# Kernel tuning notes

Hardware: AMD Instinct MI355X
Metric: run time of the kernel (lower is better)

Reference implementation:

```python
import jax, jax.numpy as jnp
import numpy as np

N_LEVELS = 2 ** 4 - 1  # 4-bit uniform quantization -> 15 intervals


def fake_quant(x, lower, upper):
    """Uniform asymmetric fake-quantization with straight-through rounding.
    clamp to [lower, upper], quantize to 4-bit grid, dequantize."""
    scale = (upper - lower) / N_LEVELS
    xc = jnp.clip(x, lower, upper)
    q = (xc - lower) / scale
    # straight-through estimator for round
    q = q + jax.lax.stop_gradient(jnp.round(q) - q)
    return q * scale + lower


def setup_inputs() -> dict:
    key = jax.random.key(0)
    kA, kB = jax.random.split(key)
    A = jax.random.normal(kA, (128, 8, 256, 64), dtype=jnp.float32)
    B = jax.random.normal(kB, (128, 8, 64, 256), dtype=jnp.float32)
    # learnable per-tensor bounds (as found by init_quantization_scale search)
    a_lower = jnp.full((1,), -2.5, dtype=jnp.float32)
    a_upper = jnp.full((1,), 2.5, dtype=jnp.float32)
    b_lower = jnp.full((1,), -2.5, dtype=jnp.float32)
    b_upper = jnp.full((1,), 2.5, dtype=jnp.float32)
    return {"A": A, "B": B, "a_lower": a_lower, "a_upper": a_upper,
            "b_lower": b_lower, "b_upper": b_upper}


def reference(A, B, a_lower, a_upper, b_lower, b_upper):
    Aq = fake_quant(A, a_lower, a_upper)
    Bq = fake_quant(B, b_lower, b_upper)
    # batched matmul: [bw, h, n, d] @ [bw, h, d, n] -> [bw, h, n, n]
    return jnp.einsum('bhnd,bhdm->bhnm', Aq, Bq)
```

## Files before the change

### kernel.cpp

```cpp
#include <hip/hip_runtime.h>

typedef __attribute__((ext_vector_type(4))) int   int4v;
typedef __attribute__((ext_vector_type(4))) float float4v;

__device__ __forceinline__ int swz(int row, int slot) {
    return slot ^ ((row ^ (row >> 2)) & 3);
}

__device__ __forceinline__ int quant1(float x, float lo, float up, float scale) {
    float xc = fminf(fmaxf(x, lo), up);
    return (int)rintf((xc - lo) / scale);
}

__device__ __forceinline__ int qpack4(float4v v, float lo, float up, float sc) {
    return  quant1(v[0], lo, up, sc)        | (quant1(v[1], lo, up, sc) << 8) |
           (quant1(v[2], lo, up, sc) << 16) | (quant1(v[3], lo, up, sc) << 24);
}

__device__ __forceinline__ unsigned bsum(int p) {
    return ((unsigned)p * 0x01010101u) >> 24;
}

__global__ __launch_bounds__(256, 4) void qmm_kernel(
    const float* __restrict__ A, const float* __restrict__ B,
    const float* __restrict__ aLo, const float* __restrict__ aUp,
    const float* __restrict__ bLo, const float* __restrict__ bUp,
    float* __restrict__ Out)
{
    __shared__ int   qB[256 * 16];
    __shared__ float CBf[256];

    const int tid = threadIdx.x;
    const int b   = blockIdx.x;

    const float lA = aLo[0], uA = aUp[0];
    const float lB = bLo[0], uB = bUp[0];
    const float sA  = (uA - lA) / 15.0f;
    const float sB  = (uB - lB) / 15.0f;
    const float sAB = sA * sB;

    const float4v* A4 = (const float4v*)(A + (size_t)b * 256 * 64);
    const float4v* B4 = (const float4v*)(B + (size_t)b * 64 * 256);
    float* outb = Out + (size_t)b * 256 * 256;

    {
        const int u = tid & 63, w = tid >> 6;
        int pk[4][4];
        #pragma unroll
        for (int m = 0; m < 4; ++m) {
            float4v r0 = __builtin_nontemporal_load(&B4[(size_t)(w*16 + m*4 + 0) * 64 + u]);
            float4v r1 = __builtin_nontemporal_load(&B4[(size_t)(w*16 + m*4 + 1) * 64 + u]);
            float4v r2 = __builtin_nontemporal_load(&B4[(size_t)(w*16 + m*4 + 2) * 64 + u]);
            float4v r3 = __builtin_nontemporal_load(&B4[(size_t)(w*16 + m*4 + 3) * 64 + u]);
            #pragma unroll
            for (int c = 0; c < 4; ++c) {
                pk[c][m] =  quant1(r0[c], lB, uB, sB)        | (quant1(r1[c], lB, uB, sB) << 8) |
                           (quant1(r2[c], lB, uB, sB) << 16) | (quant1(r3[c], lB, uB, sB) << 24);
            }
        }
        #pragma unroll
        for (int c = 0; c < 4; ++c) {
            int col = u * 4 + c;
            int4v v = {pk[c][0], pk[c][1], pk[c][2], pk[c][3]};
            *(int4v*)&qB[col * 16 + swz(col, w) * 4] = v;
        }
    }
    __syncthreads();

    {
        unsigned s = 0;
        #pragma unroll
        for (int sl = 0; sl < 4; ++sl) {
            int4v v = *(const int4v*)&qB[tid * 16 + swz(tid, sl) * 4];
            s += bsum(v[0]) + bsum(v[1]) + bsum(v[2]) + bsum(v[3]);
        }
        CBf[tid] = lA * sB * (float)s;
    }

    const int lane = tid & 63, wave = tid >> 6;
    const int lr = lane & 15, lk = lane >> 4;
    const float c64 = 64.0f * lA * lB;

    int4v afrag[4];
    float RA[4];
    #pragma unroll
    for (int rt = 0; rt < 4; ++rt) {
        int row = wave * 64 + rt * 16 + lr;
        const float4v* ap = A4 + (size_t)row * 16 + lk * 4;
        float4v x0 = __builtin_nontemporal_load(ap + 0);
        float4v x1 = __builtin_nontemporal_load(ap + 1);
        float4v x2 = __builtin_nontemporal_load(ap + 2);
        float4v x3 = __builtin_nontemporal_load(ap + 3);
        int p0 = qpack4(x0, lA, uA, sA), p1 = qpack4(x1, lA, uA, sA);
        int p2 = qpack4(x2, lA, uA, sA), p3 = qpack4(x3, lA, uA, sA);
        int4v f = {p0, p1, p2, p3};
        afrag[rt] = f;
        int rs = (int)(bsum(p0) + bsum(p1) + bsum(p2) + bsum(p3));
        rs += __shfl_xor(rs, 16);
        rs += __shfl_xor(rs, 32);
        RA[rt] = sA * lB * (float)rs + c64;
    }
    __syncthreads();

    const int4v z4 = {0, 0, 0, 0};
    #pragma unroll 2
    for (int ct = 0; ct < 16; ++ct) {
        int col = ct * 16 + lr;
        int4v  bfrag = *(const int4v*)&qB[col * 16 + swz(col, lk) * 4];
        float4v cb   = *(const float4v*)&CBf[ct * 16 + lk * 4];
        #pragma unroll
        for (int rt = 0; rt < 4; ++rt) {
            int4v acc = __builtin_amdgcn_mfma_i32_16x16x64_i8(bfrag, afrag[rt], z4, 0, 0, 0);
            int row = wave * 64 + rt * 16 + lr;
            float4v o;
            o[0] = fmaf(sAB, (float)acc[0], RA[rt] + cb[0]);
            o[1] = fmaf(sAB, (float)acc[1], RA[rt] + cb[1]);
            o[2] = fmaf(sAB, (float)acc[2], RA[rt] + cb[2]);
            o[3] = fmaf(sAB, (float)acc[3], RA[rt] + cb[3]);
            __builtin_nontemporal_store(o, (float4v*)&outb[(size_t)row * 256 + ct * 16 + lk * 4]);
        }
    }
}

extern "C" void kernel_launch(void* const* d_in, const int* in_sizes, int n_in,
                              void* d_out, int out_size, void* d_ws, size_t ws_size,
                              hipStream_t stream) {
    const float* A   = (const float*)d_in[0];
    const float* B   = (const float*)d_in[1];
    const float* aLo = (const float*)d_in[2];
    const float* aUp = (const float*)d_in[3];
    const float* bLo = (const float*)d_in[4];
    const float* bUp = (const float*)d_in[5];
    float* Out = (float*)d_out;

    int batches = in_sizes[0] / (256 * 64);
    qmm_kernel<<<batches, 256, 0, stream>>>(A, B, aLo, aUp, bLo, bUp, Out);
}
```

Before: 121.2 us.

## Stage quantized A through LDS with coalesced loads and precomputed row sums

A is now loaded with fully coalesced flat float4 loads, quantized, and stored to a swizzled LDS tile. Row sums for A and column sums for B are computed from LDS, replacing the per-fragment strided global loads and cross-lane shuffles. B's LDS layout becomes a per-k-slot int4 array with an XOR column permutation, and the output loop unroll goes from 2 to 4. Nontemporal loads and stores are swapped for ordinary ones, which changes cache behaviour on a kernel dominated by output writes. In exchange there is an extra barrier and more LDS use, which may lower occupancy.

```diff
diff --git a/kernel.cpp b/kernel.cpp
--- a/kernel.cpp
+++ b/kernel.cpp
@@ -7,14 +7,13 @@
     return slot ^ ((row ^ (row >> 2)) & 3);
 }
 
+__device__ __forceinline__ int pcol(int col) {
+    return col ^ ((col >> 3) & 7);
+}
+
 __device__ __forceinline__ int quant1(float x, float lo, float up, float scale) {
     float xc = fminf(fmaxf(x, lo), up);
     return (int)rintf((xc - lo) / scale);
-}
-
-__device__ __forceinline__ int qpack4(float4v v, float lo, float up, float sc) {
-    return  quant1(v[0], lo, up, sc)        | (quant1(v[1], lo, up, sc) << 8) |
-           (quant1(v[2], lo, up, sc) << 16) | (quant1(v[3], lo, up, sc) << 24);
 }
 
 __device__ __forceinline__ unsigned bsum(int p) {
@@ -27,7 +26,9 @@
     const float* __restrict__ bLo, const float* __restrict__ bUp,
     float* __restrict__ Out)
 {
-    __shared__ int   qB[256 * 16];
+    __shared__ int   qA[256 * 16];
+    __shared__ int4v qB16[4][256];
+    __shared__ float RAf[256];
     __shared__ float CBf[256];
 
     const int tid = threadIdx.x;
@@ -43,15 +44,28 @@
     const float4v* B4 = (const float4v*)(B + (size_t)b * 64 * 256);
     float* outb = Out + (size_t)b * 256 * 256;
 
+    #pragma unroll
+    for (int it = 0; it < 16; ++it) {
+        int f = it * 256 + tid;
+        float4v v = A4[f];
+        int q0 = quant1(v[0], lA, uA, sA);
+        int q1 = quant1(v[1], lA, uA, sA);
+        int q2 = quant1(v[2], lA, uA, sA);
+        int q3 = quant1(v[3], lA, uA, sA);
+        int p  = q0 | (q1 << 8) | (q2 << 16) | (q3 << 24);
+        int row = f >> 4, chunk = f & 15;
+        qA[row * 16 + swz(row, chunk >> 2) * 4 + (chunk & 3)] = p;
+    }
+
     {
         const int u = tid & 63, w = tid >> 6;
         int pk[4][4];
         #pragma unroll
         for (int m = 0; m < 4; ++m) {
-            float4v r0 = __builtin_nontemporal_load(&B4[(size_t)(w*16 + m*4 + 0) * 64 + u]);
-            float4v r1 = __builtin_nontemporal_load(&B4[(size_t)(w*16 + m*4 + 1) * 64 + u]);
-            float4v r2 = __builtin_nontemporal_load(&B4[(size_t)(w*16 + m*4 + 2) * 64 + u]);
-            float4v r3 = __builtin_nontemporal_load(&B4[(size_t)(w*16 + m*4 + 3) * 64 + u]);
+            float4v r0 = B4[(size_t)(w*16 + m*4 + 0) * 64 + u];
+            float4v r1 = B4[(size_t)(w*16 + m*4 + 1) * 64 + u];
+            float4v r2 = B4[(size_t)(w*16 + m*4 + 2) * 64 + u];
+            float4v r3 = B4[(size_t)(w*16 + m*4 + 3) * 64 + u];
             #pragma unroll
             for (int c = 0; c < 4; ++c) {
                 pk[c][m] =  quant1(r0[c], lB, uB, sB)        | (quant1(r1[c], lB, uB, sB) << 8) |
@@ -62,52 +76,43 @@
         for (int c = 0; c < 4; ++c) {
             int col = u * 4 + c;
             int4v v = {pk[c][0], pk[c][1], pk[c][2], pk[c][3]};
-            *(int4v*)&qB[col * 16 + swz(col, w) * 4] = v;
+            qB16[w][pcol(col)] = v;
         }
     }
     __syncthreads();
 
     {
-        unsigned s = 0;
+        unsigned sa = 0, sb = 0;
         #pragma unroll
         for (int sl = 0; sl < 4; ++sl) {
-            int4v v = *(const int4v*)&qB[tid * 16 + swz(tid, sl) * 4];
-            s += bsum(v[0]) + bsum(v[1]) + bsum(v[2]) + bsum(v[3]);
+            int4v va = *(const int4v*)&qA[tid * 16 + swz(tid, sl) * 4];
+            int4v vb = qB16[sl][pcol(tid)];
+            sa += bsum(va[0]) + bsum(va[1]) + bsum(va[2]) + bsum(va[3]);
+            sb += bsum(vb[0]) + bsum(vb[1]) + bsum(vb[2]) + bsum(vb[3]);
         }
-        CBf[tid] = lA * sB * (float)s;
+        float c32 = 32.0f * lA * lB;
+        RAf[tid] = sA * lB * (float)sa + c32;
+        CBf[tid] = lA * sB * (float)sb + c32;
     }
+    __syncthreads();
 
     const int lane = tid & 63, wave = tid >> 6;
     const int lr = lane & 15, lk = lane >> 4;
-    const float c64 = 64.0f * lA * lB;
 
     int4v afrag[4];
     float RA[4];
     #pragma unroll
     for (int rt = 0; rt < 4; ++rt) {
         int row = wave * 64 + rt * 16 + lr;
-        const float4v* ap = A4 + (size_t)row * 16 + lk * 4;
-        float4v x0 = __builtin_nontemporal_load(ap + 0);
-        float4v x1 = __builtin_nontemporal_load(ap + 1);
-        float4v x2 = __builtin_nontemporal_load(ap + 2);
-        float4v x3 = __builtin_nontemporal_load(ap + 3);
-        int p0 = qpack4(x0, lA, uA, sA), p1 = qpack4(x1, lA, uA, sA);
-        int p2 = qpack4(x2, lA, uA, sA), p3 = qpack4(x3, lA, uA, sA);
-        int4v f = {p0, p1, p2, p3};
-        afrag[rt] = f;
-        int rs = (int)(bsum(p0) + bsum(p1) + bsum(p2) + bsum(p3));
-        rs += __shfl_xor(rs, 16);
-        rs += __shfl_xor(rs, 32);
-        RA[rt] = sA * lB * (float)rs + c64;
+        afrag[rt] = *(const int4v*)&qA[row * 16 + swz(row, lk) * 4];
+        RA[rt]    = RAf[row];
     }
-    __syncthreads();
 
     const int4v z4 = {0, 0, 0, 0};
-    #pragma unroll 2
+    #pragma unroll 4
     for (int ct = 0; ct < 16; ++ct) {
-        int col = ct * 16 + lr;
-        int4v  bfrag = *(const int4v*)&qB[col * 16 + swz(col, lk) * 4];
-        float4v cb   = *(const float4v*)&CBf[ct * 16 + lk * 4];
+        int4v   bfrag = qB16[lk][pcol(ct * 16 + lr)];
+        float4v cb    = *(const float4v*)&CBf[ct * 16 + lk * 4];
         #pragma unroll
         for (int rt = 0; rt < 4; ++rt) {
             int4v acc = __builtin_amdgcn_mfma_i32_16x16x64_i8(bfrag, afrag[rt], z4, 0, 0, 0);
@@ -117,7 +122,7 @@
             o[1] = fmaf(sAB, (float)acc[1], RA[rt] + cb[1]);
             o[2] = fmaf(sAB, (float)acc[2], RA[rt] + cb[2]);
             o[3] = fmaf(sAB, (float)acc[3], RA[rt] + cb[3]);
-            __builtin_nontemporal_store(o, (float4v*)&outb[(size_t)row * 256 + ct * 16 + lk * 4]);
+            *(float4v*)&outb[(size_t)row * 256 + ct * 16 + lk * 4] = o;
         }
     }
 }
```

Result: slower. 125.2 us (+3.3%).
